# Kernel tuning notes

Measured on AMD Instinct MI355X. Metric: run time of the kernel, lower is better.

Reference implementation:

```python
import jax, jax.numpy as jnp
import numpy as np

STATE_DIM = 128
N_STATES = 4096
N_ACTIONS = 512
D = 16384  # random_feature_dim
B = 16     # batch of parallel episodes
ALPHA = 1.0
BETA = 1.0
SQRT_D = np.sqrt(D).astype(np.float32)


def _phi(W, x):
    """RandomFeatureMap: exp(1j * W @ x / alpha) / sqrt(D).
    W: [D, state_dim] real (torch randn .to(complex64) has zero imag part).
    x: [..., state_dim] real -> returns complex64 [..., D].
    """
    z = jnp.einsum('di,...i->...d', W, x) / ALPHA  # real phase
    return jax.lax.complex(jnp.cos(z), jnp.sin(z)) / SQRT_D


def setup_inputs() -> dict:
    key = jax.random.key(0)
    k1, k2, k3, k4, k5 = jax.random.split(key, 5)
    obs = jax.random.uniform(k1, (B, N_STATES), dtype=jnp.float32)
    action = jax.random.uniform(k2, (B, N_ACTIONS), dtype=jnp.float32)
    Q = jax.random.normal(k3, (STATE_DIM, N_STATES), dtype=jnp.float32) / np.sqrt(STATE_DIM).astype(np.float32)
    V = jax.random.normal(k4, (STATE_DIM, N_ACTIONS), dtype=jnp.float32) / np.sqrt(STATE_DIM).astype(np.float32)
    W = jax.random.normal(k5, (D, STATE_DIM), dtype=jnp.float32) / ALPHA
    return {"obs": obs, "action": action, "Q": Q, "V": V, "W": W}


def reference(obs, action, Q, V, W):
    # phi_Q = random_feature_map(Q.T).T : [D, n_states], also the memory M
    phi_Q = _phi(W, Q.T).T                                  # [D, S] complex64
    # get_state_from_memory: state = M @ obs
    state = phi_Q @ obs.T.astype(jnp.complex64)             # [D, B]
    # clean_up: weights = softmax(beta * Re(phi_Q^H @ state)); new_state = phi_Q @ weights
    scores = BETA * jnp.real(phi_Q.conj().T @ state)        # [S, B]
    weights = jax.nn.softmax(scores, axis=0)
    new_state = phi_Q @ weights.astype(jnp.complex64)       # [D, B]
    # update_state: state *= phi(V @ action)
    v = V @ action.T                                        # [state_dim, B]
    phi_v = _phi(W, v.T).T                                  # [D, B]
    out_state = new_state * phi_v
    # get_obs_from_memory: softmax(beta * Re(M^H @ state))
    out_scores = jax.nn.softmax(BETA * jnp.real(phi_Q.conj().T @ out_state), axis=0)  # [S, B]
    return out_scores
```

## Files before the change

### kernel.cpp

```cpp
#include <hip/hip_runtime.h>
#include <hip/hip_bf16.h>
#include <cstdint>
#include <cstddef>

#define D_DIM 16384
#define S_DIM 4096
#define A_DIM 512
#define K_DIM 128
#define B_DIM 16
#define CH    16

#define INV2PI 0.15915494309189535f

typedef float f32x4 __attribute__((ext_vector_type(4)));
typedef short s16x8 __attribute__((ext_vector_type(8)));
typedef unsigned short u16;
typedef unsigned int   u32;

__device__ __forceinline__ u16 bf16bits(float x) {
    return __builtin_bit_cast(u16, (__bf16)x);
}
__device__ __forceinline__ s16x8 frag_cast(uint4 u) {
    return __builtin_bit_cast(s16x8, u);
}
__device__ __forceinline__ u32 cvt_pk_bf16(float lo, float hi) {
    u32 r;
    asm("v_cvt_pk_bf16_f32 %0, %1, %2" : "=v"(r) : "v"(lo), "v"(hi));
    return r;
}
__device__ __forceinline__ int sigma(int row) {
    return (row & 7) ^ ((row >> 1) & 4);
}
__device__ __forceinline__ void g2l16(const u32* g, u32* l) {
    __builtin_amdgcn_global_load_lds((const __attribute__((address_space(1))) u32*)g,
                                     (__attribute__((address_space(3))) u32*)l, 16, 0, 0);
}
template<int N> __device__ __forceinline__ void vwait() {
    asm volatile("s_waitcnt vmcnt(%0)" :: "n"(N) : "memory");
}

__global__ void prep_kernel(const float* __restrict__ W, const float* __restrict__ Q,
                            const float* __restrict__ obs,
                            u16* __restrict__ Wb, u16* __restrict__ QT, u16* __restrict__ obsP)
{
    const int i0 = blockIdx.x * 256 + threadIdx.x;
    const int stride = gridDim.x * 256;
    const float4* wp = (const float4*)W;
    for (int i = i0; i < D_DIM * 16; i += stride) {
        float4 a = wp[2 * i], b = wp[2 * i + 1];
        uint4 o;
        o.x = cvt_pk_bf16(a.x * INV2PI, a.y * INV2PI);
        o.y = cvt_pk_bf16(a.z * INV2PI, a.w * INV2PI);
        o.z = cvt_pk_bf16(b.x * INV2PI, b.y * INV2PI);
        o.w = cvt_pk_bf16(b.z * INV2PI, b.w * INV2PI);
        ((uint4*)Wb)[i] = o;
    }
    for (int i = i0; i < S_DIM * 16; i += stride) {
        const int s = i >> 4, kc = i & 15;
        float q[8];
        #pragma unroll
        for (int j = 0; j < 8; ++j) q[j] = Q[(size_t)(kc * 8 + j) * S_DIM + s];
        uint4 o;
        o.x = cvt_pk_bf16(q[0], q[1]);
        o.y = cvt_pk_bf16(q[2], q[3]);
        o.z = cvt_pk_bf16(q[4], q[5]);
        o.w = cvt_pk_bf16(q[6], q[7]);
        ((uint4*)QT)[s * 16 + kc] = o;
    }
    for (int i = i0; i < B_DIM * S_DIM; i += stride) {
        int b = i >> 12, s = i & 4095;
        obsP[((s >> 3) << 7) + (b << 3) + (s & 7)] = bf16bits(obs[i]);
    }
}

__global__ void kv_kernel(const float* __restrict__ V, const float* __restrict__ act,
                          float* __restrict__ v)
{
    const int t = threadIdx.x;
    const int out = blockIdx.x * 32 + (t >> 3);
    const int part = t & 7;
    const int k = out >> 4, b = out & 15;
    const float4* vp = (const float4*)(V + (size_t)k * A_DIM);
    const float4* ap = (const float4*)(act + (size_t)b * A_DIM);
    float s = 0.f;
    #pragma unroll
    for (int q = part * 16; q < part * 16 + 16; ++q) {
        float4 x = vp[q], y = ap[q];
        s += x.x * y.x + x.y * y.y + x.z * y.z + x.w * y.w;
    }
    s += __shfl_xor(s, 1, 64);
    s += __shfl_xor(s, 2, 64);
    s += __shfl_xor(s, 4, 64);
    if (part == 0) v[out] = s;
}

__global__ void phiv_kernel(const float* __restrict__ W, const float* __restrict__ v,
                            float* __restrict__ pvr, float* __restrict__ pvi)
{
    __shared__ float sv[K_DIM * 16];
    const int tid = threadIdx.x;
    for (int j = tid; j < K_DIM * 16; j += 256) sv[j] = v[j];
    __syncthreads();
    const int i = blockIdx.x * 256 + tid;
    const int d = i >> 4, b = i & 15;
    const float4* wp = (const float4*)(W + (size_t)d * K_DIM);
    float z = 0.f;
    #pragma unroll 8
    for (int q = 0; q < 32; ++q) {
        float4 w4 = wp[q];
        z += w4.x * sv[(4 * q + 0) * 16 + b] + w4.y * sv[(4 * q + 1) * 16 + b]
           + w4.z * sv[(4 * q + 2) * 16 + b] + w4.w * sv[(4 * q + 3) * 16 + b];
    }
    pvr[i] = cosf(z) * 0.0078125f;
    pvi[i] = sinf(z) * 0.0078125f;
}

template<int MODE>
__global__ __launch_bounds__(256, 2)
void fused_pass(const u16* __restrict__ P1, const u16* __restrict__ P2,
                const u16* __restrict__ y1, const u16* __restrict__ y2,
                float* __restrict__ out1, float* __restrict__ out2, int Mrows)
{
    __shared__ u32 lds[4][4096];
    const int tid = threadIdx.x;
    const int w   = tid >> 6;
    const int l   = tid & 63;
    const int n0  = l & 15;
    const int hi  = l >> 4;
    const int wm  = w & 1;
    const int wk  = w >> 1;
    const int m0  = blockIdx.x * 64 + wm * 32;
    const int kbase0 = blockIdx.y * (CH * 64);

    s16x8 bfrag[2][4];
    #pragma unroll
    for (int mt = 0; mt < 2; ++mt) {
        const uint4* ap = (const uint4*)(P1 + (size_t)(m0 + 16 * mt + n0) * 128);
        #pragma unroll
        for (int ki = 0; ki < 4; ++ki) bfrag[mt][ki] = frag_cast(ap[4 * ki + hi]);
    }

    int gofs[4];
    #pragma unroll
    for (int i = 0; i < 4; ++i) {
        const int row = 16 * w + 4 * i + hi;
        gofs[i] = row * 128 + ((n0 ^ sigma(row)) << 3);
    }
    const u16* p2base = P2 + (size_t)kbase0 * 128;

    #define STAGE(c, b) { \
        const u16* src_ = p2base + (size_t)(c) * 64 * 128; \
        _Pragma("unroll") \
        for (int i_ = 0; i_ < 4; ++i_) \
            g2l16((const u32*)(src_ + gofs[i_]), &lds[b][w * 1024 + i_ * 256]); }

    const size_t ybase = (size_t)(4 * wk + hi) * 128 + (size_t)n0 * 8;
    #define YLD(Y, c) (*(const uint4*)((Y) + (size_t)((kbase0 + (c) * 64) >> 3) * 128 + ybase))

    f32x4 acc1[2] = {{0.f,0.f,0.f,0.f},{0.f,0.f,0.f,0.f}};
    f32x4 acc2[2] = {{0.f,0.f,0.f,0.f},{0.f,0.f,0.f,0.f}};

    const int rowT0 = 32 * wk + 8 * (n0 >> 2) + (n0 & 3);

    STAGE(0, 0);
    uint4 y1c = YLD(y1, 0);
    uint4 y2c;
    if (MODE == 1) y2c = YLD(y2, 0);
    STAGE(1, 1);

    #pragma unroll 1
    for (int c = 0; c < CH; ++c) {
        uint4 y1n, y2n;
        if (c < CH - 1) {
            y1n = YLD(y1, c + 1);
            if (MODE == 1) y2n = YLD(y2, c + 1);
        }
        if (c < CH - 2) {
            STAGE(c + 2, (c + 2) & 3);
            vwait<8 + ((MODE == 1) ? 2 : 1)>();
        } else if (c == CH - 2) {
            vwait<4 + ((MODE == 1) ? 2 : 1)>();
        } else {
            vwait<0>();
        }
        __builtin_amdgcn_s_barrier();
        __builtin_amdgcn_sched_barrier(0);

        const u32* buf = lds[c & 3];
        u32 cf0[4], sf0[4], cf1[4], sf1[4];
        #pragma unroll
        for (int T = 0; T < 2; ++T) {
            const int row = rowT0 + 4 * T;
            const int sg  = sigma(row);
            const u32* rb = buf + row * 64;
            uint4 af[4];
            #pragma unroll
            for (int ki = 0; ki < 4; ++ki)
                af[ki] = *(const uint4*)(rb + (((4 * ki + hi) ^ sg) << 2));
            f32x4 z0 = {0.f,0.f,0.f,0.f}, z1 = {0.f,0.f,0.f,0.f};
            #pragma unroll
            for (int ki = 0; ki < 4; ++ki) {
                z0 = __builtin_amdgcn_mfma_f32_16x16x32_bf16(frag_cast(af[ki]), bfrag[0][ki], z0, 0, 0, 0);
                z1 = __builtin_amdgcn_mfma_f32_16x16x32_bf16(frag_cast(af[ki]), bfrag[1][ki], z1, 0, 0, 0);
            }
            float c0[4], s0[4], c1[4], s1[4];
            #pragma unroll
            for (int r = 0; r < 4; ++r) {
                const float rv0 = __builtin_amdgcn_fractf(z0[r]);
                c0[r] = __builtin_amdgcn_cosf(rv0);
                s0[r] = __builtin_amdgcn_sinf(rv0);
                const float rv1 = __builtin_amdgcn_fractf(z1[r]);
                c1[r] = __builtin_amdgcn_cosf(rv1);
                s1[r] = __builtin_amdgcn_sinf(rv1);
            }
            cf0[2 * T + 0] = cvt_pk_bf16(c0[0], c0[1]);
            cf0[2 * T + 1] = cvt_pk_bf16(c0[2], c0[3]);
            sf0[2 * T + 0] = cvt_pk_bf16(s0[0], s0[1]);
            sf0[2 * T + 1] = cvt_pk_bf16(s0[2], s0[3]);
            cf1[2 * T + 0] = cvt_pk_bf16(c1[0], c1[1]);
            cf1[2 * T + 1] = cvt_pk_bf16(c1[2], c1[3]);
            sf1[2 * T + 0] = cvt_pk_bf16(s1[0], s1[1]);
            sf1[2 * T + 1] = cvt_pk_bf16(s1[2], s1[3]);
        }
        const s16x8 cfr0 = frag_cast(uint4{cf0[0], cf0[1], cf0[2], cf0[3]});
        const s16x8 sfr0 = frag_cast(uint4{sf0[0], sf0[1], sf0[2], sf0[3]});
        const s16x8 cfr1 = frag_cast(uint4{cf1[0], cf1[1], cf1[2], cf1[3]});
        const s16x8 sfr1 = frag_cast(uint4{sf1[0], sf1[1], sf1[2], sf1[3]});
        const s16x8 yf1 = frag_cast(y1c);
        if (MODE == 0) {
            acc1[0] = __builtin_amdgcn_mfma_f32_16x16x32_bf16(cfr0, yf1, acc1[0], 0, 0, 0);
            acc2[0] = __builtin_amdgcn_mfma_f32_16x16x32_bf16(sfr0, yf1, acc2[0], 0, 0, 0);
            acc1[1] = __builtin_amdgcn_mfma_f32_16x16x32_bf16(cfr1, yf1, acc1[1], 0, 0, 0);
            acc2[1] = __builtin_amdgcn_mfma_f32_16x16x32_bf16(sfr1, yf1, acc2[1], 0, 0, 0);
        } else {
            const s16x8 yf2 = frag_cast(y2c);
            acc1[0] = __builtin_amdgcn_mfma_f32_16x16x32_bf16(cfr0, yf1, acc1[0], 0, 0, 0);
            acc1[0] = __builtin_amdgcn_mfma_f32_16x16x32_bf16(sfr0, yf2, acc1[0], 0, 0, 0);
            acc1[1] = __builtin_amdgcn_mfma_f32_16x16x32_bf16(cfr1, yf1, acc1[1], 0, 0, 0);
            acc1[1] = __builtin_amdgcn_mfma_f32_16x16x32_bf16(sfr1, yf2, acc1[1], 0, 0, 0);
        }
        if (c < CH - 1) {
            y1c = y1n;
            if (MODE == 1) y2c = y2n;
        }
    }
    #undef STAGE
    #undef YLD

    float* red = reinterpret_cast<float*>(&lds[0][0]);
    if (wk == 1) {
        #pragma unroll
        for (int mt = 0; mt < 2; ++mt)
            #pragma unroll
            for (int r = 0; r < 4; ++r) {
                red[((wm * 2 + mt) * 16 + 4 * hi + r) * 16 + n0] = acc1[mt][r];
                if (MODE == 0)
                    red[1024 + ((wm * 2 + mt) * 16 + 4 * hi + r) * 16 + n0] = acc2[mt][r];
            }
    }
    __syncthreads();
    if (wk == 0) {
        float* o1 = out1 + (size_t)blockIdx.y * Mrows * 16;
        float* o2 = out2 + (size_t)blockIdx.y * Mrows * 16;
        #pragma unroll
        for (int mt = 0; mt < 2; ++mt)
            #pragma unroll
            for (int r = 0; r < 4; ++r) {
                const int orow = m0 + 16 * mt + 4 * hi + r;
                const float v1 = acc1[mt][r] + red[((wm * 2 + mt) * 16 + 4 * hi + r) * 16 + n0];
                if (MODE == 0) {
                    o1[orow * 16 + n0] = v1;
                    o2[orow * 16 + n0] = acc2[mt][r] + red[1024 + ((wm * 2 + mt) * 16 + 4 * hi + r) * 16 + n0];
                } else {
                    o1[(size_t)n0 * Mrows + orow] = v1;
                }
            }
    }
}

__global__ void finishA(const float* __restrict__ ar, const float* __restrict__ ai,
                        u16* __restrict__ pr, u16* __restrict__ pi)
{
    const int i = blockIdx.x * 256 + threadIdx.x;
    float sr = 0.f, si = 0.f;
    #pragma unroll
    for (int p = 0; p < 4; ++p) {
        sr += ar[(size_t)p * (D_DIM * 16) + i];
        si += ai[(size_t)p * (D_DIM * 16) + i];
    }
    const int d = i >> 4, b = i & 15;
    const int pidx = ((d >> 3) << 7) + (b << 3) + (d & 7);
    pr[pidx] = bf16bits(sr * 0.0078125f);
    pi[pidx] = bf16bits(si * 0.0078125f);
}

__global__ void finishC(const float* __restrict__ ar, const float* __restrict__ ai,
                        const float* __restrict__ pvr, const float* __restrict__ pvi,
                        u16* __restrict__ pr, u16* __restrict__ pi)
{
    const int i = blockIdx.x * 256 + threadIdx.x;
    float sr = 0.f, si = 0.f;
    #pragma unroll
    for (int p = 0; p < 4; ++p) {
        sr += ar[(size_t)p * (D_DIM * 16) + i];
        si += ai[(size_t)p * (D_DIM * 16) + i];
    }
    const float nr = sr * 0.0078125f, ni = si * 0.0078125f;
    const float xr = nr * pvr[i] - ni * pvi[i];
    const float xi = nr * pvi[i] + ni * pvr[i];
    const int d = i >> 4, b = i & 15;
    const int pidx = ((d >> 3) << 7) + (b << 3) + (d & 7);
    pr[pidx] = bf16bits(xr);
    pi[pidx] = bf16bits(xi);
}

template<int OUT>
__global__ void softmax_col(const float* __restrict__ acc, u16* __restrict__ wp,
                            float* __restrict__ outp)
{
    const int b = blockIdx.x;
    const int tid = threadIdx.x;
    __shared__ float red[4];
    float4 x[4];
    float m = -1e30f;
    #pragma unroll
    for (int j = 0; j < 4; ++j) {
        float4 s4 = {0.f, 0.f, 0.f, 0.f};
        #pragma unroll
        for (int p = 0; p < 16; ++p) {
            const float4 t = *(const float4*)(acc + (size_t)p * (S_DIM * 16)
                                              + (size_t)b * S_DIM + (j * 256 + tid) * 4);
            s4.x += t.x; s4.y += t.y; s4.z += t.z; s4.w += t.w;
        }
        x[j].x = s4.x * 0.0078125f; x[j].y = s4.y * 0.0078125f;
        x[j].z = s4.z * 0.0078125f; x[j].w = s4.w * 0.0078125f;
        m = fmaxf(fmaxf(m, fmaxf(x[j].x, x[j].y)), fmaxf(x[j].z, x[j].w));
    }
    #pragma unroll
    for (int off = 1; off < 64; off <<= 1) m = fmaxf(m, __shfl_xor(m, off, 64));
    if ((tid & 63) == 0) red[tid >> 6] = m;
    __syncthreads();
    m = fmaxf(fmaxf(red[0], red[1]), fmaxf(red[2], red[3]));
    float sum = 0.f;
    #pragma unroll
    for (int j = 0; j < 4; ++j) {
        x[j].x = expf(x[j].x - m); x[j].y = expf(x[j].y - m);
        x[j].z = expf(x[j].z - m); x[j].w = expf(x[j].w - m);
        sum += x[j].x + x[j].y + x[j].z + x[j].w;
    }
    #pragma unroll
    for (int off = 1; off < 64; off <<= 1) sum += __shfl_xor(sum, off, 64);
    __syncthreads();
    if ((tid & 63) == 0) red[tid >> 6] = sum;
    __syncthreads();
    const float inv = 1.0f / (red[0] + red[1] + red[2] + red[3]);
    #pragma unroll
    for (int j = 0; j < 4; ++j) {
        const int s4i = (j * 256 + tid) * 4;
        float v4[4] = {x[j].x * inv, x[j].y * inv, x[j].z * inv, x[j].w * inv};
        #pragma unroll
        for (int q = 0; q < 4; ++q) {
            const int s = s4i + q;
            if (OUT == 0) wp[((s >> 3) << 7) + (b << 3) + (s & 7)] = bf16bits(v4[q]);
            else          outp[s * 16 + b] = v4[q];
        }
    }
}

extern "C" void kernel_launch(void* const* d_in, const int* in_sizes, int n_in,
                              void* d_out, int out_size, void* d_ws, size_t ws_size,
                              hipStream_t stream)
{
    const float* obs = (const float*)d_in[0];
    const float* act = (const float*)d_in[1];
    const float* Q   = (const float*)d_in[2];
    const float* V   = (const float*)d_in[3];
    const float* W   = (const float*)d_in[4];
    float* out = (float*)d_out;
    char* ws = (char*)d_ws;

    u16*   Wb     = (u16*)  (ws + 0);
    u16*   QT     = (u16*)  (ws + 4194304);
    u16*   obsP   = (u16*)  (ws + 5242880);
    u16*   wP     = (u16*)  (ws + 5373952);
    u16*   stRe   = (u16*)  (ws + 5505024);
    u16*   stIm   = (u16*)  (ws + 6029312);
    u16*   osRe   = (u16*)  (ws + 6553600);
    u16*   osIm   = (u16*)  (ws + 7077888);
    float* pvR    = (float*)(ws + 7602176);
    float* pvI    = (float*)(ws + 8650752);
    float* vv     = (float*)(ws + 9699328);
    float* partR  = (float*)(ws + 9707520);
    float* partI  = (float*)(ws + 18096128);
    float* partS  = (float*)(ws + 9707520);

    prep_kernel<<<1024, 256, 0, stream>>>(W, Q, obs, Wb, QT, obsP);
    kv_kernel<<<64, 256, 0, stream>>>(V, act, vv);
    phiv_kernel<<<1024, 256, 0, stream>>>(W, vv, pvR, pvI);

    fused_pass<0><<<dim3(256, 4), 256, 0, stream>>>(Wb, QT, obsP, obsP, partR, partI, D_DIM);
    finishA<<<1024, 256, 0, stream>>>(partR, partI, stRe, stIm);

    fused_pass<1><<<dim3(64, 16), 256, 0, stream>>>(QT, Wb, stRe, stIm, partS, partS, S_DIM);
    softmax_col<0><<<16, 256, 0, stream>>>(partS, wP, nullptr);

    fused_pass<0><<<dim3(256, 4), 256, 0, stream>>>(Wb, QT, wP, wP, partR, partI, D_DIM);
    finishC<<<1024, 256, 0, stream>>>(partR, partI, pvR, pvI, osRe, osIm);

    fused_pass<1><<<dim3(64, 16), 256, 0, stream>>>(QT, Wb, osRe, osIm, partS, partS, S_DIM);
    softmax_col<1><<<16, 256, 0, stream>>>(partS, nullptr, out);
}
```

Before: 242.5 us.

## Merge prep kernels, tile phiv via LDS, switch fused pass to double buffering

Result: faster. 226.7 us (-6.5%).

```diff
diff --git a/kernel.cpp b/kernel.cpp
--- a/kernel.cpp
+++ b/kernel.cpp
@@ -35,93 +35,104 @@
     __builtin_amdgcn_global_load_lds((const __attribute__((address_space(1))) u32*)g,
                                      (__attribute__((address_space(3))) u32*)l, 16, 0, 0);
 }
-template<int N> __device__ __forceinline__ void vwait() {
-    asm volatile("s_waitcnt vmcnt(%0)" :: "n"(N) : "memory");
-}
-
-__global__ void prep_kernel(const float* __restrict__ W, const float* __restrict__ Q,
-                            const float* __restrict__ obs,
-                            u16* __restrict__ Wb, u16* __restrict__ QT, u16* __restrict__ obsP)
-{
-    const int i0 = blockIdx.x * 256 + threadIdx.x;
-    const int stride = gridDim.x * 256;
-    const float4* wp = (const float4*)W;
-    for (int i = i0; i < D_DIM * 16; i += stride) {
-        float4 a = wp[2 * i], b = wp[2 * i + 1];
-        uint4 o;
-        o.x = cvt_pk_bf16(a.x * INV2PI, a.y * INV2PI);
-        o.y = cvt_pk_bf16(a.z * INV2PI, a.w * INV2PI);
-        o.z = cvt_pk_bf16(b.x * INV2PI, b.y * INV2PI);
-        o.w = cvt_pk_bf16(b.z * INV2PI, b.w * INV2PI);
-        ((uint4*)Wb)[i] = o;
-    }
-    for (int i = i0; i < S_DIM * 16; i += stride) {
-        const int s = i >> 4, kc = i & 15;
-        float q[8];
-        #pragma unroll
-        for (int j = 0; j < 8; ++j) q[j] = Q[(size_t)(kc * 8 + j) * S_DIM + s];
-        uint4 o;
-        o.x = cvt_pk_bf16(q[0], q[1]);
-        o.y = cvt_pk_bf16(q[2], q[3]);
-        o.z = cvt_pk_bf16(q[4], q[5]);
-        o.w = cvt_pk_bf16(q[6], q[7]);
-        ((uint4*)QT)[s * 16 + kc] = o;
-    }
-    for (int i = i0; i < B_DIM * S_DIM; i += stride) {
-        int b = i >> 12, s = i & 4095;
-        obsP[((s >> 3) << 7) + (b << 3) + (s & 7)] = bf16bits(obs[i]);
-    }
-}
-
-__global__ void kv_kernel(const float* __restrict__ V, const float* __restrict__ act,
-                          float* __restrict__ v)
-{
-    const int t = threadIdx.x;
-    const int out = blockIdx.x * 32 + (t >> 3);
-    const int part = t & 7;
-    const int k = out >> 4, b = out & 15;
-    const float4* vp = (const float4*)(V + (size_t)k * A_DIM);
-    const float4* ap = (const float4*)(act + (size_t)b * A_DIM);
-    float s = 0.f;
-    #pragma unroll
-    for (int q = part * 16; q < part * 16 + 16; ++q) {
-        float4 x = vp[q], y = ap[q];
-        s += x.x * y.x + x.y * y.y + x.z * y.z + x.w * y.w;
-    }
-    s += __shfl_xor(s, 1, 64);
-    s += __shfl_xor(s, 2, 64);
-    s += __shfl_xor(s, 4, 64);
-    if (part == 0) v[out] = s;
-}
-
-__global__ void phiv_kernel(const float* __restrict__ W, const float* __restrict__ v,
-                            float* __restrict__ pvr, float* __restrict__ pvi)
-{
-    __shared__ float sv[K_DIM * 16];
+
+__global__ __launch_bounds__(256, 4)
+void prep_kernel(const float* __restrict__ W, const float* __restrict__ Q,
+                 const float* __restrict__ obs, const float* __restrict__ V,
+                 const float* __restrict__ act,
+                 u16* __restrict__ Wb, u16* __restrict__ QT,
+                 u16* __restrict__ obsP, float* __restrict__ vv)
+{
+    __shared__ float tsp[32][257];
     const int tid = threadIdx.x;
-    for (int j = tid; j < K_DIM * 16; j += 256) sv[j] = v[j];
-    __syncthreads();
-    const int i = blockIdx.x * 256 + tid;
-    const int d = i >> 4, b = i & 15;
-    const float4* wp = (const float4*)(W + (size_t)d * K_DIM);
+    if (blockIdx.x < 1024) {
+        const int i0 = blockIdx.x * 256 + tid;
+        const int stride = 1024 * 256;
+        const float4* wp = (const float4*)W;
+        for (int i = i0; i < D_DIM * 16; i += stride) {
+            float4 a = wp[2 * i], b = wp[2 * i + 1];
+            uint4 o;
+            o.x = cvt_pk_bf16(a.x * INV2PI, a.y * INV2PI);
+            o.y = cvt_pk_bf16(a.z * INV2PI, a.w * INV2PI);
+            o.z = cvt_pk_bf16(b.x * INV2PI, b.y * INV2PI);
+            o.w = cvt_pk_bf16(b.z * INV2PI, b.w * INV2PI);
+            ((uint4*)Wb)[i] = o;
+        }
+        for (int i = i0; i < B_DIM * S_DIM; i += stride) {
+            int b = i >> 12, s = i & 4095;
+            obsP[((s >> 3) << 7) + (b << 3) + (s & 7)] = bf16bits(obs[i]);
+        }
+    } else if (blockIdx.x < 1088) {
+        const int out = (blockIdx.x - 1024) * 32 + (tid >> 3);
+        const int part = tid & 7;
+        const int k = out >> 4, b = out & 15;
+        const float4* vp = (const float4*)(V + (size_t)k * A_DIM);
+        const float4* ap = (const float4*)(act + (size_t)b * A_DIM);
+        float s = 0.f;
+        #pragma unroll
+        for (int q = part * 16; q < part * 16 + 16; ++q) {
+            float4 x = vp[q], y = ap[q];
+            s += x.x * y.x + x.y * y.y + x.z * y.z + x.w * y.w;
+        }
+        s += __shfl_xor(s, 1, 64);
+        s += __shfl_xor(s, 2, 64);
+        s += __shfl_xor(s, 4, 64);
+        if (part == 0) vv[out] = s;
+    } else {
+        const int idx = blockIdx.x - 1088;
+        const int k0 = (idx & 3) * 32;
+        const int s0 = (idx >> 2) * 256;
+        #pragma unroll 4
+        for (int r = 0; r < 32; ++r)
+            tsp[r][tid] = Q[(size_t)(k0 + r) * S_DIM + s0 + tid];
+        __syncthreads();
+        u16* dst = QT + (size_t)(s0 + tid) * 128 + k0;
+        #pragma unroll
+        for (int j = 0; j < 4; ++j) {
+            uint4 o;
+            o.x = cvt_pk_bf16(tsp[8 * j + 0][tid], tsp[8 * j + 1][tid]);
+            o.y = cvt_pk_bf16(tsp[8 * j + 2][tid], tsp[8 * j + 3][tid]);
+            o.z = cvt_pk_bf16(tsp[8 * j + 4][tid], tsp[8 * j + 5][tid]);
+            o.w = cvt_pk_bf16(tsp[8 * j + 6][tid], tsp[8 * j + 7][tid]);
+            *(uint4*)(dst + 8 * j) = o;
+        }
+    }
+}
+
+__global__ __launch_bounds__(256, 4)
+void phiv_kernel(const float* __restrict__ W, const float* __restrict__ v,
+                 float* __restrict__ pvr, float* __restrict__ pvi)
+{
+    __shared__ float wl[16][132];
+    __shared__ float svT[16][132];
+    const int tid = threadIdx.x;
+    const int d0 = blockIdx.x * 16;
+    for (int j = tid; j < 2048; j += 256)
+        wl[j >> 7][j & 127] = W[(size_t)d0 * 128 + j];
+    for (int j = tid; j < 2048; j += 256)
+        svT[j & 15][j >> 4] = v[j];
+    __syncthreads();
+    const int dd = tid >> 4, b = tid & 15;
     float z = 0.f;
-    #pragma unroll 8
+    #pragma unroll
     for (int q = 0; q < 32; ++q) {
-        float4 w4 = wp[q];
-        z += w4.x * sv[(4 * q + 0) * 16 + b] + w4.y * sv[(4 * q + 1) * 16 + b]
-           + w4.z * sv[(4 * q + 2) * 16 + b] + w4.w * sv[(4 * q + 3) * 16 + b];
-    }
-    pvr[i] = cosf(z) * 0.0078125f;
-    pvi[i] = sinf(z) * 0.0078125f;
+        const float4 w4 = *(const float4*)&wl[dd][4 * q];
+        const float4 s4 = *(const float4*)&svT[b][4 * q];
+        z += w4.x * s4.x + w4.y * s4.y + w4.z * s4.z + w4.w * s4.w;
+    }
+    const float rv = __builtin_amdgcn_fractf(z * INV2PI);
+    const int i = (d0 + dd) * 16 + b;
+    pvr[i] = __builtin_amdgcn_cosf(rv) * 0.0078125f;
+    pvi[i] = __builtin_amdgcn_sinf(rv) * 0.0078125f;
 }
 
 template<int MODE>
-__global__ __launch_bounds__(256, 2)
+__global__ __launch_bounds__(256, 4)
 void fused_pass(const u16* __restrict__ P1, const u16* __restrict__ P2,
                 const u16* __restrict__ y1, const u16* __restrict__ y2,
                 float* __restrict__ out1, float* __restrict__ out2, int Mrows)
 {
-    __shared__ u32 lds[4][4096];
+    __shared__ u32 lds[2][4096];
     const int tid = threadIdx.x;
     const int w   = tid >> 6;
     const int l   = tid & 63;
@@ -143,50 +154,41 @@
     int gofs[4];
     #pragma unroll
     for (int i = 0; i < 4; ++i) {
-        const int row = 16 * w + 4 * i + hi;
-        gofs[i] = row * 128 + ((n0 ^ sigma(row)) << 3);
+        const int row = 16 * w + 4 * i + (l >> 4);
+        gofs[i] = row * 128 + (((l & 15) ^ sigma(row)) << 3);
     }
     const u16* p2base = P2 + (size_t)kbase0 * 128;
 
-    #define STAGE(c, b) { \
-        const u16* src_ = p2base + (size_t)(c) * 64 * 128; \
-        _Pragma("unroll") \
-        for (int i_ = 0; i_ < 4; ++i_) \
-            g2l16((const u32*)(src_ + gofs[i_]), &lds[b][w * 1024 + i_ * 256]); }
+    f32x4 acc1[2] = {{0.f,0.f,0.f,0.f},{0.f,0.f,0.f,0.f}};
+    f32x4 acc2[2] = {{0.f,0.f,0.f,0.f},{0.f,0.f,0.f,0.f}};
+
+    const int rowT0 = 32 * wk + 8 * (n0 >> 2) + (n0 & 3);
 
     const size_t ybase = (size_t)(4 * wk + hi) * 128 + (size_t)n0 * 8;
     #define YLD(Y, c) (*(const uint4*)((Y) + (size_t)((kbase0 + (c) * 64) >> 3) * 128 + ybase))
 
-    f32x4 acc1[2] = {{0.f,0.f,0.f,0.f},{0.f,0.f,0.f,0.f}};
-    f32x4 acc2[2] = {{0.f,0.f,0.f,0.f},{0.f,0.f,0.f,0.f}};
-
-    const int rowT0 = 32 * wk + 8 * (n0 >> 2) + (n0 & 3);
-
-    STAGE(0, 0);
+    {
+        #pragma unroll
+        for (int i = 0; i < 4; ++i)
+            g2l16((const u32*)(p2base + gofs[i]), &lds[0][w * 1024 + i * 256]);
+    }
     uint4 y1c = YLD(y1, 0);
     uint4 y2c;
     if (MODE == 1) y2c = YLD(y2, 0);
-    STAGE(1, 1);
+    __syncthreads();
 
     #pragma unroll 1
     for (int c = 0; c < CH; ++c) {
         uint4 y1n, y2n;
         if (c < CH - 1) {
+            const u16* src = p2base + (size_t)(c + 1) * 64 * 128;
+            #pragma unroll
+            for (int i = 0; i < 4; ++i)
+                g2l16((const u32*)(src + gofs[i]), &lds[(c + 1) & 1][w * 1024 + i * 256]);
             y1n = YLD(y1, c + 1);
             if (MODE == 1) y2n = YLD(y2, c + 1);
         }
-        if (c < CH - 2) {
-            STAGE(c + 2, (c + 2) & 3);
-            vwait<8 + ((MODE == 1) ? 2 : 1)>();
-        } else if (c == CH - 2) {
-            vwait<4 + ((MODE == 1) ? 2 : 1)>();
-        } else {
-            vwait<0>();
-        }
-        __builtin_amdgcn_s_barrier();
-        __builtin_amdgcn_sched_barrier(0);
-
-        const u32* buf = lds[c & 3];
+        const u32* buf = lds[c & 1];
         u32 cf0[4], sf0[4], cf1[4], sf1[4];
         #pragma unroll
         for (int T = 0; T < 2; ++T) {
@@ -239,12 +241,12 @@
             acc1[1] = __builtin_amdgcn_mfma_f32_16x16x32_bf16(cfr1, yf1, acc1[1], 0, 0, 0);
             acc1[1] = __builtin_amdgcn_mfma_f32_16x16x32_bf16(sfr1, yf2, acc1[1], 0, 0, 0);
         }
+        __syncthreads();
         if (c < CH - 1) {
             y1c = y1n;
             if (MODE == 1) y2c = y2n;
         }
     }
-    #undef STAGE
     #undef YLD
 
     float* red = reinterpret_cast<float*>(&lds[0][0]);
@@ -394,8 +396,7 @@
     float* partI  = (float*)(ws + 18096128);
     float* partS  = (float*)(ws + 9707520);
 
-    prep_kernel<<<1024, 256, 0, stream>>>(W, Q, obs, Wb, QT, obsP);
-    kv_kernel<<<64, 256, 0, stream>>>(V, act, vv);
+    prep_kernel<<<1152, 256, 0, stream>>>(W, Q, obs, V, act, Wb, QT, obsP, vv);
     phiv_kernel<<<1024, 256, 0, stream>>>(W, vv, pvR, pvI);
 
     fused_pass<0><<<dim3(256, 4), 256, 0, stream>>>(Wb, QT, obsP, obsP, partR, partI, D_DIM);
```
